# Optimization experiments

Measured on AMD Instinct MI355X. Metric: run time of the kernel, lower is better.

## Reference

```python
import jax, jax.numpy as jnp
import numpy as np

TAU = 2.0
THR = 1.0
ALPHA = 10.0
FLOW_SCALE = 16.0  # 2 ** flow_scale_pow2 (=4)
DECAY = 1.0 - 1.0 / TAU


def conv2d(x, w, b=None, stride=1, pad=0):
    # x: [N,C,H,W], w: [O,I,kh,kw]
    out = jax.lax.conv_general_dilated(
        x, w, (stride, stride), [(pad, pad), (pad, pad)],
        dimension_numbers=('NCHW', 'OIHW', 'NCHW'))
    if b is not None:
        out = out + b[None, :, None, None]
    return out


@jax.custom_vjp
def spike(v):
    return (v > 0).astype(v.dtype)

def _spike_fwd(v):
    return (v > 0).astype(v.dtype), v

def _spike_bwd(v, g):
    s = jax.nn.sigmoid(ALPHA * v)
    return (g * ALPHA * s * (1.0 - s),)

spike.defvjp(_spike_fwd, _spike_bwd)


def lif(x, w, b, mem, stride, pad):
    """Conv + leaky-integrate-fire with soft reset. mem init 0 -> first step mem=cur."""
    cur = conv2d(x, w, b, stride, pad)
    mem = mem * DECAY + cur
    s = spike(mem - THR)
    mem = mem - s * THR
    return s, mem


def up2(x):
    return jnp.repeat(jnp.repeat(x, 2, axis=2), 2, axis=3)


def forward(x, w_e1, b_e1, w_e2, b_e2, w_e3, b_e3, w_d3, b_d3,
            w_d2, b_d2, w_d1, b_d1, w_skip2, w_skip1, w_flow, b_flow):
    N, T, C, H, W = x.shape
    bc = w_e1.shape[0]  # base_ch = 32
    z = lambda c, h, w: jnp.zeros((N, c, h, w), x.dtype)
    init = (
        z(bc, H // 2, W // 2),      # mem_e1
        z(2 * bc, H // 4, W // 4),  # mem_e2
        z(4 * bc, H // 8, W // 8),  # mem_e3
        z(2 * bc, H // 4, W // 4),  # mem_d3
        z(bc, H // 2, W // 2),      # mem_d2
        z(bc, H, W),                # mem_d1
        z(bc, H // 2, W // 2),      # mean_e1 (zeros + /(t+1) rule == None-init)
        z(2 * bc, H // 4, W // 4),  # mean_e2
        z(2, H, W),                 # flow_mean
    )

    def step(carry, inp):
        t, xt = inp
        m1, m2, m3, md3, md2, md1, me1, me2, fm = carry
        s1, m1 = lif(xt, w_e1, b_e1, m1, 2, 2)
        s2, m2 = lif(s1, w_e2, b_e2, m2, 2, 1)
        s3, m3 = lif(s2, w_e3, b_e3, m3, 2, 1)
        tf = (t + 1).astype(xt.dtype)
        me1 = me1 + (s1 - me1) / tf
        me2 = me2 + (s2 - me2) / tf
        d3, md3 = lif(up2(s3), w_d3, b_d3, md3, 1, 1)
        d3 = d3 + conv2d(me2, w_skip2)
        d2, md2 = lif(up2(d3), w_d2, b_d2, md2, 1, 1)
        d2 = d2 + conv2d(me1, w_skip1)
        d1, md1 = lif(up2(d2), w_d1, b_d1, md1, 1, 1)
        flow = conv2d(d1, w_flow, b_flow, 1, 1) * FLOW_SCALE
        fm = fm + (flow - fm) / tf
        return (m1, m2, m3, md3, md2, md1, me1, me2, fm), flow

    _, flows = jax.lax.scan(step, init, (jnp.arange(T), jnp.moveaxis(x, 1, 0)))
    return flows[-1]  # return_last_flow=True -> flow of final timestep [N,2,H,W]


def setup_inputs() -> dict:
    key = jax.random.key(0)
    ks = jax.random.split(key, 16)
    N, T, H, W, bc = 4, 8, 256, 256, 32

    def w(k, o, i, kh, kw):
        return jax.random.normal(k, (o, i, kh, kw), jnp.float32) / np.sqrt(i * kh * kw)

    return {
        'x': jax.random.uniform(ks[0], (N, T, 2, H, W), jnp.float32),
        'w_e1': w(ks[1], bc, 2, 5, 5), 'b_e1': jnp.zeros((bc,), jnp.float32),
        'w_e2': w(ks[2], 2 * bc, bc, 3, 3), 'b_e2': jnp.zeros((2 * bc,), jnp.float32),
        'w_e3': w(ks[3], 4 * bc, 2 * bc, 3, 3), 'b_e3': jnp.zeros((4 * bc,), jnp.float32),
        'w_d3': w(ks[4], 2 * bc, 4 * bc, 3, 3), 'b_d3': jnp.zeros((2 * bc,), jnp.float32),
        'w_d2': w(ks[5], bc, 2 * bc, 3, 3), 'b_d2': jnp.zeros((bc,), jnp.float32),
        'w_d1': w(ks[6], bc, bc, 3, 3), 'b_d1': jnp.zeros((bc,), jnp.float32),
        'w_skip2': w(ks[7], 2 * bc, 2 * bc, 1, 1),
        'w_skip1': w(ks[8], bc, bc, 1, 1),
        'w_flow': w(ks[9], 2, bc, 3, 3), 'b_flow': jnp.zeros((2,), jnp.float32),
    }


def reference(x, w_e1, b_e1, w_e2, b_e2, w_e3, b_e3, w_d3, b_d3,
              w_d2, b_d2, w_d1, b_d1, w_skip2, w_skip1, w_flow, b_flow):
    return forward(x, w_e1, b_e1, w_e2, b_e2, w_e3, b_e3, w_d3, b_d3,
                   w_d2, b_d2, w_d1, b_d1, w_skip2, w_skip1, w_flow, b_flow)
```

## Files before the change

### kernel.cpp

```cpp
#include <hip/hip_runtime.h>
#include <cstdint>
#include <cstddef>


static constexpr float THRc   = 1.0f;
static constexpr float DECAYc = 0.5f;

__device__ __forceinline__ float getc(const float4& v, int k) {
    switch (k & 3) {
        case 0: return v.x;
        case 1: return v.y;
        case 2: return v.z;
        default: return v.w;
    }
}

__global__ __launch_bounds__(256) void prep_collapse(const float* __restrict__ w,
                                                     float* __restrict__ wc, int pairs)
{
    int idx = blockIdx.x * 256 + threadIdx.x;
    if (idx >= pairs) return;
    float a[3][3];
#pragma unroll
    for (int i = 0; i < 3; ++i)
#pragma unroll
        for (int j = 0; j < 3; ++j) a[i][j] = w[idx * 9 + i * 3 + j];
    float rs[2][2][3];
#pragma unroll
    for (int kx = 0; kx < 3; ++kx) {
        rs[0][0][kx] = a[0][kx];
        rs[0][1][kx] = a[1][kx] + a[2][kx];
        rs[1][0][kx] = a[0][kx] + a[1][kx];
        rs[1][1][kx] = a[2][kx];
    }
#pragma unroll
    for (int py = 0; py < 2; ++py)
#pragma unroll
        for (int px = 0; px < 2; ++px)
#pragma unroll
            for (int r = 0; r < 2; ++r) {
                float c0, c1;
                if (px == 0) { c0 = rs[py][r][0];               c1 = rs[py][r][1] + rs[py][r][2]; }
                else         { c0 = rs[py][r][0] + rs[py][r][1]; c1 = rs[py][r][2]; }
                wc[idx * 16 + ((py * 2 + px) * 2 + r) * 2 + 0] = c0;
                wc[idx * 16 + ((py * 2 + px) * 2 + r) * 2 + 1] = c1;
            }
}

template<int IC, int ICC, int OC, int SIH, int SIW, int CPT, int YPB, int OCT,
         int NW, int SKIP_IC, int SKC>
__device__ __forceinline__ void dec_conv_body(
    int b, float* __restrict__ sb,
    const float* __restrict__ in,
    const float* __restrict__ wc,
    const float* __restrict__ bias,
    float* __restrict__ mem,
    float* __restrict__ out,
    const float* __restrict__ skip_in,
    const float* __restrict__ skip_w)
{
    constexpr int NT   = NW * 64;
    constexpr int LPT  = SIW / CPT;
    static_assert((CPT & 1) == 0 && (CPT == 2 || (CPT & 3) == 0), "CPT even");
    static_assert(LPT * YPB == 64, "wave must tile the band");
    static_assert((ICC & 1) == 0, "ICC even");
    constexpr int OC_B = NW * OCT;
    constexpr int NOCB = OC / OC_B;
    constexpr int NYB  = SIH / YPB;
    constexpr int SP   = SIW + 8;
    constexpr int SR   = YPB + 2;
    constexpr int OH   = 2 * SIH, OW = 2 * SIW;
    constexpr int NCH  = IC / ICC;
    constexpr int W4   = SIW / 4;
    constexpr int TILE = ICC * SR * SP;
    constexpr int OROWS = 2 * YPB;
    constexpr int SLOTS = ICC * SR * W4;

    const int ocb = b % NOCB; b /= NOCB;
    const int yb  = b % NYB;  b /= NYB;
    const int n   = b;
    const int y0  = yb * YPB;

    const int lane = threadIdx.x & 63;
    const int wav  = threadIdx.x >> 6;
    const int cl   = lane % LPT;
    const int yp   = lane / LPT;
    const int c0   = cl * CPT;
    const int y    = y0 + yp;

    const int oc0 = __builtin_amdgcn_readfirstlane(ocb * OC_B + wav * OCT);

    int lzero;
    asm volatile("v_mov_b32 %0, 0" : "=v"(lzero));
    const float4* wlane = reinterpret_cast<const float4*>(wc) + lzero;
    const int wbase = oc0 * IC * 4;

    for (int f = threadIdx.x; f < 2 * ICC * SR * 2; f += NT) {
        int side = f & 1;
        int t    = f >> 1;
        int r    = t % SR;
        int tt   = t / SR;
        int ic   = tt % ICC;
        int buf  = tt / ICC;
        sb[buf * TILE + (ic * SR + r) * SP + (side ? (SIW + 4) : 3)] = 0.0f;
    }

    float acc[OCT][2][2 * CPT];
#pragma unroll
    for (int j = 0; j < OCT; ++j) {
        float bv = bias[oc0 + j];
#pragma unroll
        for (int py = 0; py < 2; ++py)
#pragma unroll
            for (int q = 0; q < 2 * CPT; ++q) acc[j][py][q] = bv;
    }

    const float* inn = in + (size_t)n * IC * SIH * SIW;

    float4 wA[OCT * 4], wB[OCT * 4];
    auto wload = [&](int icg, float4* dst) {
#pragma unroll
        for (int j = 0; j < OCT; ++j)
#pragma unroll
            for (int g = 0; g < 4; ++g)
                dst[j * 4 + g] = wlane[wbase + (j * IC + icg) * 4 + g];
    };

    auto stage = [&](int buf, int ch) {
        const float* inb = inn + (size_t)ch * ICC * SIH * SIW;
        float* dst = sb + buf * TILE;
        for (int f = threadIdx.x; f < SLOTS; f += NT) {
            int c4 = f & (W4 - 1);
            int t  = f / W4;
            int r  = t % SR;
            int ic = t / SR;
            int sy = y0 - 1 + r;
            float4 v = make_float4(0.f, 0.f, 0.f, 0.f);
            if (sy >= 0 && sy < SIH)
                v = *reinterpret_cast<const float4*>(
                        inb + (size_t)ic * SIH * SIW + (size_t)sy * SIW + 4 * c4);
            *reinterpret_cast<float4*>(&dst[(ic * SR + r) * SP + 4 + 4 * c4]) = v;
        }
    };

    auto compute = [&](const float* bp, int icl, const float4* w) {
        float s[3][CPT + 2];
#pragma unroll
        for (int r = 0; r < 3; ++r) {
            const int rb = (icl * SR + yp + r) * SP;
            s[r][0] = bp[rb + 3 + c0];
            if constexpr (CPT >= 4) {
#pragma unroll
                for (int v = 0; v < CPT / 4; ++v) {
                    float4 t4 = *reinterpret_cast<const float4*>(&bp[rb + 4 + c0 + 4 * v]);
                    s[r][1 + 4 * v] = t4.x; s[r][2 + 4 * v] = t4.y;
                    s[r][3 + 4 * v] = t4.z; s[r][4 + 4 * v] = t4.w;
                }
            } else {
                float2 t2 = *reinterpret_cast<const float2*>(&bp[rb + 4 + c0]);
                s[r][1] = t2.x; s[r][2] = t2.y;
            }
            s[r][CPT + 1] = bp[rb + 4 + c0 + CPT];
        }
#pragma unroll
        for (int j = 0; j < OCT; ++j)
#pragma unroll
            for (int py = 0; py < 2; ++py)
#pragma unroll
                for (int cc = 0; cc < CPT; ++cc)
#pragma unroll
                    for (int px = 0; px < 2; ++px) {
                        float v = acc[j][py][cc * 2 + px];
#pragma unroll
                        for (int rr = 0; rr < 2; ++rr)
#pragma unroll
                            for (int c2 = 0; c2 < 2; ++c2)
                                v += getc(w[j * 4 + py * 2 + px], rr * 2 + c2)
                                   * s[py + rr][cc + px + c2];
                        acc[j][py][cc * 2 + px] = v;
                    }
    };

    wload(0, wA);
    stage(0, 0);
    __syncthreads();
    for (int ch = 0; ch < NCH; ++ch) {
        if (ch + 1 < NCH) stage((ch + 1) & 1, ch + 1);
        const float* bp = sb + (ch & 1) * TILE;
        const int icg0 = ch * ICC;
        for (int ic = 0; ic < ICC; ic += 2) {
            wload(icg0 + ic + 1, wB);
            compute(bp, ic, wA);
            wload(icg0 + ic + 2, wA);
            compute(bp, ic + 1, wB);
        }
        __syncthreads();
    }

    constexpr int NV = (2 * CPT) / 4;
    float sk[OCT][2][2 * CPT] = {};
    if constexpr (SKIP_IC > 0) {
        constexpr int NSK = SKIP_IC / SKC;
        constexpr int OW4 = OW / 4;
        const float* skn = skip_in + (size_t)n * SKIP_IC * OH * OW;
        for (int sc = 0; sc < NSK; ++sc) {
            if (sc) __syncthreads();
            for (int f = threadIdx.x; f < SKC * OROWS * OW4; f += NT) {
                int c4 = f & (OW4 - 1);
                int t  = f / OW4;
                int r  = t % OROWS;
                int ic = t / OROWS;
                *reinterpret_cast<float4*>(&sb[(ic * OROWS + r) * OW + 4 * c4]) =
                    *reinterpret_cast<const float4*>(
                        skn + ((size_t)(sc * SKC + ic) * OH + 2 * y0 + r) * OW + 4 * c4);
            }
            __syncthreads();
            float wsk[OCT][SKC];
#pragma unroll
            for (int j = 0; j < OCT; ++j)
#pragma unroll
                for (int ic = 0; ic < SKC; ++ic)
                    wsk[j][ic] = skip_w[(size_t)(oc0 + j) * SKIP_IC + sc * SKC + ic];
#pragma unroll
            for (int ic = 0; ic < SKC; ++ic)
#pragma unroll
                for (int py = 0; py < 2; ++py)
#pragma unroll
                    for (int v = 0; v < NV; ++v) {
                        float4 sv = *reinterpret_cast<const float4*>(
                            &sb[(ic * OROWS + 2 * yp + py) * OW + 2 * c0 + 4 * v]);
#pragma unroll
                        for (int j = 0; j < OCT; ++j) {
                            sk[j][py][4 * v + 0] += wsk[j][ic] * sv.x;
                            sk[j][py][4 * v + 1] += wsk[j][ic] * sv.y;
                            sk[j][py][4 * v + 2] += wsk[j][ic] * sv.z;
                            sk[j][py][4 * v + 3] += wsk[j][ic] * sv.w;
                        }
                    }
        }
    }

    const bool wout = (out != nullptr);
#pragma unroll
    for (int j = 0; j < OCT; ++j)
#pragma unroll
        for (int py = 0; py < 2; ++py) {
            size_t ob = (((size_t)n * OC + oc0 + j) * OH + (2 * y + py)) * OW + 2 * c0;
#pragma unroll
            for (int v = 0; v < NV; ++v) {
                float4 mv = *reinterpret_cast<const float4*>(&mem[ob + 4 * v]);
                float4 ov, nm;
                float m0 = mv.x * DECAYc + acc[j][py][4 * v + 0];
                float m1 = mv.y * DECAYc + acc[j][py][4 * v + 1];
                float m2 = mv.z * DECAYc + acc[j][py][4 * v + 2];
                float m3 = mv.w * DECAYc + acc[j][py][4 * v + 3];
                float s0 = (m0 - THRc) > 0.0f ? 1.0f : 0.0f;
                float s1 = (m1 - THRc) > 0.0f ? 1.0f : 0.0f;
                float s2 = (m2 - THRc) > 0.0f ? 1.0f : 0.0f;
                float s3 = (m3 - THRc) > 0.0f ? 1.0f : 0.0f;
                nm.x = m0 - s0 * THRc; nm.y = m1 - s1 * THRc;
                nm.z = m2 - s2 * THRc; nm.w = m3 - s3 * THRc;
                *reinterpret_cast<float4*>(&mem[ob + 4 * v]) = nm;
                if (wout) {
                    ov.x = s0 + sk[j][py][4 * v + 0];
                    ov.y = s1 + sk[j][py][4 * v + 1];
                    ov.z = s2 + sk[j][py][4 * v + 2];
                    ov.w = s3 + sk[j][py][4 * v + 3];
                    *reinterpret_cast<float4*>(&out[ob + 4 * v]) = ov;
                }
            }
        }
}

template<int IC, int ICC, int OC, int IH, int IW, int K, int CPT, int LPT, int OCT, bool DO_MEAN>
__device__ __forceinline__ void enc_conv_body(
    int b, float* __restrict__ sb,
    const float* __restrict__ in, int in_nstride,
    const float* __restrict__ wgt, const float* __restrict__ bias,
    float* __restrict__ mem, float* __restrict__ out,
    const float* __restrict__ mean_in, float* __restrict__ mean_out, float inv_tf)
{
    constexpr int P    = K / 2;
    constexpr int OH   = IH / 2, OW = IW / 2;
    constexpr int SPr  = 4 + IW + P;
    constexpr int SP   = (SPr + 3) & ~3;
    constexpr int OC_B = 4 * OCT;
    constexpr int NOCB = OC / OC_B;
    constexpr int RL   = 2 * CPT + 2 * P - 1;
    constexpr int NCH  = IC / ICC;
    constexpr int W4   = IW / 4;
    static_assert(LPT * CPT == OW, "lanes x CPT must cover OW");
    static_assert((ICC & (ICC - 1)) == 0, "ICC pow2");

    const int ocb = b % NOCB; b /= NOCB;
    const int y   = b % OH;   b /= OH;
    const int n   = b;

    const int lane = threadIdx.x & 63;
    const int wav  = threadIdx.x >> 6;
    const int x0   = (lane % LPT) * CPT;
    const int oc0  = __builtin_amdgcn_readfirstlane(ocb * OC_B + wav * OCT);

    for (int f = threadIdx.x; f < K * ICC * 2 * P; f += 256) {
        int h  = f % (2 * P);
        int t  = f / (2 * P);
        int ic = t & (ICC - 1);
        int r  = t / ICC;
        int col = (h < P) ? (4 - P + h) : (4 + IW + h - P);
        sb[(r * ICC + ic) * SP + col] = 0.0f;
    }

    float acc[OCT][CPT];
#pragma unroll
    for (int j = 0; j < OCT; ++j) {
        float bv = bias[oc0 + j];
#pragma unroll
        for (int cc = 0; cc < CPT; ++cc) acc[j][cc] = bv;
    }

    const float* inn = in + (size_t)n * (size_t)in_nstride;

    for (int ch = 0; ch < NCH; ++ch) {
        __syncthreads();
        const float* inb = inn + (size_t)ch * ICC * IH * IW;
        constexpr int SLOTS = K * ICC * W4;
        for (int f = threadIdx.x; f < SLOTS; f += 256) {
            int c4 = f & (W4 - 1);
            int t  = f / W4;
            int ic = t & (ICC - 1);
            int r  = t / ICC;
            int sy = 2 * y - P + r;
            float4 v = make_float4(0.f, 0.f, 0.f, 0.f);
            if (sy >= 0 && sy < IH)
                v = *reinterpret_cast<const float4*>(
                        inb + (size_t)ic * IH * IW + (size_t)sy * IW + 4 * c4);
            *reinterpret_cast<float4*>(&sb[(r * ICC + ic) * SP + 4 + 4 * c4]) = v;
        }
        __syncthreads();
        for (int ic = 0; ic < ICC; ++ic) {
            float s[K][RL];
#pragma unroll
            for (int r = 0; r < K; ++r)
#pragma unroll
                for (int k = 0; k < RL; ++k)
                    s[r][k] = sb[(r * ICC + ic) * SP + 4 - P + 2 * x0 + k];
            const float* wp = wgt + ((size_t)oc0 * IC + ch * ICC + ic) * (K * K);
#pragma unroll
            for (int j = 0; j < OCT; ++j) {
                float wv[K * K];
#pragma unroll
                for (int k = 0; k < K * K; ++k) wv[k] = wp[(size_t)j * IC * K * K + k];
#pragma unroll
                for (int cc = 0; cc < CPT; ++cc)
#pragma unroll
                    for (int ky = 0; ky < K; ++ky)
#pragma unroll
                        for (int kx = 0; kx < K; ++kx)
                            acc[j][cc] += wv[ky * K + kx] * s[ky][2 * cc + kx];
            }
        }
    }

    if (lane < LPT) {
#pragma unroll
        for (int j = 0; j < OCT; ++j) {
            size_t ob = (((size_t)n * OC + oc0 + j) * OH + y) * OW + x0;
#pragma unroll
            for (int cc = 0; cc < CPT; ++cc) {
                float m  = mem[ob + cc] * DECAYc + acc[j][cc];
                float sp = (m - THRc) > 0.0f ? 1.0f : 0.0f;
                mem[ob + cc] = m - sp * THRc;
                if constexpr (DO_MEAN) {
                    float mv = mean_in[ob + cc];
                    mean_out[ob + cc] = mv + (sp - mv) * inv_tf;
                }
                out[ob + cc] = sp;
            }
        }
    }
}

template<int IC, int ICC, int OC, int IH, int IW, int CPT, int LPT, int OCT, bool DO_MEAN>
__device__ __forceinline__ void enc_convdb_body(
    int b, float* __restrict__ sb,
    const float* __restrict__ in, int in_nstride,
    const float* __restrict__ wgt, const float* __restrict__ bias,
    float* __restrict__ mem, float* __restrict__ out,
    const float* __restrict__ mean_in, float* __restrict__ mean_out, float inv_tf)
{
    constexpr int K    = 3;
    constexpr int P    = 1;
    constexpr int OH   = IH / 2, OW = IW / 2;
    constexpr int SPr  = 4 + IW + P;
    constexpr int SP   = (SPr + 3) & ~3;
    constexpr int OC_B = 4 * OCT;
    constexpr int NOCB = OC / OC_B;
    constexpr int RL   = 2 * CPT + 2 * P - 1;
    constexpr int NCH  = IC / ICC;
    constexpr int W4   = IW / 4;
    constexpr int TILE = K * ICC * SP;
    constexpr int SLOTS = K * ICC * W4;
    static_assert(LPT * CPT == OW, "lanes x CPT must cover OW");
    static_assert((ICC & (ICC - 1)) == 0, "ICC pow2");
    static_assert(NCH >= 2, "dbuf needs >=2 chunks");

    const int ocb = b % NOCB; b /= NOCB;
    const int y   = b % OH;   b /= OH;
    const int n   = b;

    const int lane = threadIdx.x & 63;
    const int wav  = threadIdx.x >> 6;
    const int x0   = (lane % LPT) * CPT;
    const int oc0  = __builtin_amdgcn_readfirstlane(ocb * OC_B + wav * OCT);

    for (int f = threadIdx.x; f < 2 * K * ICC * 2 * P; f += 256) {
        int h   = f % (2 * P);
        int t   = f / (2 * P);
        int ic  = t & (ICC - 1);
        int t2  = t / ICC;
        int r   = t2 % K;
        int buf = t2 / K;
        int col = (h < P) ? (4 - P + h) : (4 + IW + h - P);
        sb[buf * TILE + (r * ICC + ic) * SP + col] = 0.0f;
    }

    float acc[OCT][CPT];
#pragma unroll
    for (int j = 0; j < OCT; ++j) {
        float bv = bias[oc0 + j];
#pragma unroll
        for (int cc = 0; cc < CPT; ++cc) acc[j][cc] = bv;
    }

    const float* inn = in + (size_t)n * (size_t)in_nstride;

    auto stage = [&](int buf, int ch) {
        const float* inb = inn + (size_t)ch * ICC * IH * IW;
        float* dst = sb + buf * TILE;
        for (int f = threadIdx.x; f < SLOTS; f += 256) {
            int c4 = f & (W4 - 1);
            int t  = f / W4;
            int ic = t & (ICC - 1);
            int r  = t / ICC;
            int sy = 2 * y - P + r;
            float4 v = make_float4(0.f, 0.f, 0.f, 0.f);
            if (sy >= 0 && sy < IH)
                v = *reinterpret_cast<const float4*>(
                        inb + (size_t)ic * IH * IW + (size_t)sy * IW + 4 * c4);
            *reinterpret_cast<float4*>(&dst[(r * ICC + ic) * SP + 4 + 4 * c4]) = v;
        }
    };

    stage(0, 0);
    __syncthreads();
    for (int ch = 0; ch < NCH; ++ch) {
        if (ch + 1 < NCH) stage((ch + 1) & 1, ch + 1);
        const float* bp = sb + (ch & 1) * TILE;
        for (int ic = 0; ic < ICC; ++ic) {
            float s[K][RL];
#pragma unroll
            for (int r = 0; r < K; ++r)
#pragma unroll
                for (int k = 0; k < RL; ++k)
                    s[r][k] = bp[(r * ICC + ic) * SP + 4 - P + 2 * x0 + k];
            const float* wp = wgt + ((size_t)oc0 * IC + ch * ICC + ic) * (K * K);
#pragma unroll
            for (int j = 0; j < OCT; ++j) {
                float wv[K * K];
#pragma unroll
                for (int k = 0; k < K * K; ++k) wv[k] = wp[(size_t)j * IC * K * K + k];
#pragma unroll
                for (int cc = 0; cc < CPT; ++cc)
#pragma unroll
                    for (int ky = 0; ky < K; ++ky)
#pragma unroll
                        for (int kx = 0; kx < K; ++kx)
                            acc[j][cc] += wv[ky * K + kx] * s[ky][2 * cc + kx];
            }
        }
        __syncthreads();
    }

    if (lane < LPT) {
#pragma unroll
        for (int j = 0; j < OCT; ++j) {
            size_t ob = (((size_t)n * OC + oc0 + j) * OH + y) * OW + x0;
#pragma unroll
            for (int cc = 0; cc < CPT; ++cc) {
                float m  = mem[ob + cc] * DECAYc + acc[j][cc];
                float sp = (m - THRc) > 0.0f ? 1.0f : 0.0f;
                mem[ob + cc] = m - sp * THRc;
                if constexpr (DO_MEAN) {
                    float mv = mean_in[ob + cc];
                    mean_out[ob + cc] = mv + (sp - mv) * inv_tf;
                }
                out[ob + cc] = sp;
            }
        }
    }
}

template<int IC, int ICC, int OC, int IH, int IW, int K, int CPT, int LPT, int OCT,
         bool DO_MEAN, int SMEMW>
__global__ __launch_bounds__(256) void enc_conv_k(
    const float* in, int ns, const float* wgt, const float* bias,
    float* mem, float* out, const float* mean_in, float* mean_out, float inv_tf)
{
    __shared__ __align__(16) float smem[SMEMW];
    enc_conv_body<IC, ICC, OC, IH, IW, K, CPT, LPT, OCT, DO_MEAN>(
        (int)blockIdx.x, smem, in, ns, wgt, bias, mem, out, mean_in, mean_out, inv_tf);
}

template<int IC, int ICC, int OC, int IH, int IW, int CPT, int LPT, int OCT,
         bool DO_MEAN, int SMEMW>
__global__ __launch_bounds__(256) void enc_convdb_k(
    const float* in, int ns, const float* wgt, const float* bias,
    float* mem, float* out, const float* mean_in, float* mean_out, float inv_tf)
{
    __shared__ __align__(16) float smem[SMEMW];
    enc_convdb_body<IC, ICC, OC, IH, IW, CPT, LPT, OCT, DO_MEAN>(
        (int)blockIdx.x, smem, in, ns, wgt, bias, mem, out, mean_in, mean_out, inv_tf);
}

__global__ __launch_bounds__(256) void fused_d3_e1(
    const float* din, const float* dwc, const float* dbias, float* dmem,
    float* dout, const float* dskip_in, const float* dskip_w,
    const float* ein, int ens, const float* ew, const float* ebias,
    float* emem, float* eout, const float* emean_in, float* emean_out, float einv)
{
    __shared__ __align__(16) float smem[7680];
    int b = (int)blockIdx.x;
    if (b < 512)
        dec_conv_body<128, 16, 64, 32, 32, 2, 4, 1, 4, 64, 8>(
            b, smem, din, dwc, dbias, dmem, dout, dskip_in, dskip_w);
    else
        enc_conv_body<2, 2, 32, 256, 256, 5, 2, 64, 2, true>(
            b - 512, smem, ein, ens, ew, ebias, emem, eout, emean_in, emean_out, einv);
}

__global__ __launch_bounds__(256) void fused_d2_e2(
    const float* din, const float* dwc, const float* dbias, float* dmem,
    float* dout, const float* dskip_in, const float* dskip_w,
    const float* ein, int ens, const float* ew, const float* ebias,
    float* emem, float* eout, const float* emean_in, float* emean_out, float einv)
{
    __shared__ __align__(16) float smem[9216];
    int b = (int)blockIdx.x;
    if (b < 512)
        dec_conv_body<64, 16, 32, 64, 64, 2, 2, 2, 4, 32, 8>(
            b, smem, din, dwc, dbias, dmem, dout, dskip_in, dskip_w);
    else
        enc_convdb_body<32, 8, 64, 128, 128, 1, 64, 2, true>(
            b - 512, smem, ein, ens, ew, ebias, emem, eout, emean_in, emean_out, einv);
}

__global__ __launch_bounds__(256) void fused_d1_e3(
    const float* din, const float* dwc, const float* dbias, float* dmem,
    float* dout,
    const float* ein, int ens, const float* ew, const float* ebias,
    float* emem, float* eout, float einv)
{
    __shared__ __align__(16) float smem[8704];
    int b = (int)blockIdx.x;
    if (b < 1024)
        dec_conv_body<32, 8, 32, 128, 128, 4, 2, 2, 4, 0, 1>(
            b, smem, din, dwc, dbias, dmem, dout, nullptr, nullptr);
    else
        enc_convdb_body<64, 16, 128, 64, 64, 1, 32, 4, false>(
            b - 1024, smem, ein, ens, ew, ebias, emem, eout, nullptr, nullptr, einv);
}

template<int IC, int OC, int IH, int IW, int OH, int OW,
         int K, int STRIDE, int PAD, bool UP2, int SKIP_IC,
         bool DO_LIF, bool DO_MEAN>
__global__ __launch_bounds__(256) void conv_fused(
    const float* __restrict__ in, int in_nstride,
    const float* __restrict__ wgt,
    const float* __restrict__ bias,
    float* __restrict__ mem,
    float* __restrict__ out,
    const float* __restrict__ skip_in,
    const float* __restrict__ skip_w,
    float* __restrict__ mean,
    float inv_tf, float outscale)
{
    constexpr int VEC  = 4;
    constexpr int OWV  = OW / VEC;
    constexpr int WSZ  = IC * K * K;
    constexpr int SIH  = UP2 ? IH / 2 : IH;
    constexpr int SIW  = UP2 ? IW / 2 : IW;
    constexpr int RLEN = (VEC - 1) * STRIDE + K;

    __shared__ float sw[WSZ];

    const int bstart = blockIdx.x * 256;
    const int oc = (bstart / (OH * OWV)) % OC;

    for (int i = threadIdx.x; i < WSZ; i += 256) sw[i] = wgt[oc * WSZ + i];
    __syncthreads();

    const int idx = bstart + threadIdx.x;
    const int wx  = idx % OWV;
    int tt        = idx / OWV;
    const int oy  = tt % OH; tt /= OH;
    tt /= OC;
    const int n   = tt;
    const int ox0 = wx * VEC;

    const float bv = bias ? bias[oc] : 0.0f;
    float acc[VEC];
#pragma unroll
    for (int v = 0; v < VEC; ++v) acc[v] = bv;

    const float* inn = in + (size_t)n * (size_t)in_nstride;

    for (int ic = 0; ic < IC; ++ic) {
        const float* inc = inn + (size_t)ic * (SIH * SIW);
#pragma unroll
        for (int ky = 0; ky < K; ++ky) {
            const int uy = oy * STRIDE + ky - PAD;
            const bool rowok = (uy >= 0) & (uy < IH);
            int sy = UP2 ? (uy >> 1) : uy;
            sy = sy < 0 ? 0 : (sy > SIH - 1 ? SIH - 1 : sy);
            const float* __restrict__ row = inc + (size_t)sy * SIW;

            float r[RLEN];
#pragma unroll
            for (int j = 0; j < RLEN; ++j) {
                const int ux = ox0 * STRIDE - PAD + j;
                const bool ok = rowok & (ux >= 0) & (ux < IW);
                int sx = UP2 ? (ux >> 1) : ux;
                sx = sx < 0 ? 0 : (sx > SIW - 1 ? SIW - 1 : sx);
                r[j] = ok ? row[sx] : 0.0f;
            }
#pragma unroll
            for (int kx = 0; kx < K; ++kx) {
                const float wv = sw[(ic * K + ky) * K + kx];
#pragma unroll
                for (int v = 0; v < VEC; ++v)
                    acc[v] += r[v * STRIDE + kx] * wv;
            }
        }
    }

    const size_t obase = ((((size_t)n * OC + oc) * OH) + oy) * (size_t)OW + ox0;
#pragma unroll
    for (int v = 0; v < VEC; ++v) out[obase + v] = acc[v] * outscale;
}

extern "C" void kernel_launch(void* const* d_in, const int* in_sizes, int n_in,
                              void* d_out, int out_size, void* d_ws, size_t ws_size,
                              hipStream_t stream)
{
    const float* x     = (const float*)d_in[0];
    const float* w_e1  = (const float*)d_in[1];
    const float* b_e1  = (const float*)d_in[2];
    const float* w_e2  = (const float*)d_in[3];
    const float* b_e2  = (const float*)d_in[4];
    const float* w_e3  = (const float*)d_in[5];
    const float* b_e3  = (const float*)d_in[6];
    const float* w_d3  = (const float*)d_in[7];
    const float* b_d3  = (const float*)d_in[8];
    const float* w_d2  = (const float*)d_in[9];
    const float* b_d2  = (const float*)d_in[10];
    const float* w_d1  = (const float*)d_in[11];
    const float* b_d1  = (const float*)d_in[12];
    const float* w_sk2 = (const float*)d_in[13];
    const float* w_sk1 = (const float*)d_in[14];
    const float* w_fl  = (const float*)d_in[15];
    const float* b_fl  = (const float*)d_in[16];
    float* outp = (float*)d_out;

    float* ws = (float*)d_ws;
    size_t off = 0;
    auto alloc = [&](size_t nelem) { float* p = ws + off; off += nelem; return p; };

    float* m1   = alloc(4UL * 32 * 128 * 128);
    float* m2   = alloc(4UL * 64 * 64 * 64);
    float* m3   = alloc(4UL * 128 * 32 * 32);
    float* md3  = alloc(4UL * 64 * 64 * 64);
    float* md2  = alloc(4UL * 32 * 128 * 128);
    float* md1  = alloc(4UL * 32 * 256 * 256);
    float* me1a = alloc(4UL * 32 * 128 * 128);
    float* me1b = alloc(4UL * 32 * 128 * 128);
    float* me2  = alloc(4UL * 64 * 64 * 64);
    const size_t zcount = off;
    float* s1  = alloc(4UL * 32 * 128 * 128);
    float* s2  = alloc(4UL * 64 * 64 * 64);
    float* s3  = alloc(4UL * 128 * 32 * 32);
    float* d3a = alloc(4UL * 64 * 64 * 64);
    float* d2a = alloc(4UL * 32 * 128 * 128);
    float* d1a = alloc(4UL * 32 * 256 * 256);
    float* wc3 = alloc(64UL * 128 * 16 + 64);
    float* wc2 = alloc(32UL * 64 * 16 + 64);
    float* wc1 = alloc(32UL * 32 * 16 + 64);
    (void)ws_size; (void)in_sizes; (void)n_in; (void)out_size;

    hipMemsetAsync(d_ws, 0, zcount * sizeof(float), stream);

    prep_collapse<<<(64 * 128 + 255) / 256, 256, 0, stream>>>(w_d3, wc3, 64 * 128);
    prep_collapse<<<(32 * 64 + 255) / 256, 256, 0, stream>>>(w_d2, wc2, 32 * 64);
    prep_collapse<<<(32 * 32 + 255) / 256, 256, 0, stream>>>(w_d1, wc1, 32 * 32);

    float* me1buf[2] = { me1a, me1b };

    enc_conv_k<2, 2, 32, 256, 256, 5, 2, 64, 2, true, 2640>
        <<<4 * 128 * 4, 256, 0, stream>>>(x, 8 * 2 * 256 * 256, w_e1, b_e1,
                                          m1, s1, me1buf[0], me1buf[1], 1.0f);
    enc_convdb_k<32, 8, 64, 128, 128, 1, 64, 2, true, 6528>
        <<<4 * 64 * 8, 256, 0, stream>>>(s1, 32 * 128 * 128, w_e2, b_e2,
                                         m2, s2, me2, me2, 1.0f);
    enc_convdb_k<64, 16, 128, 64, 64, 1, 32, 4, false, 6912>
        <<<4 * 32 * 8, 256, 0, stream>>>(s2, 64 * 64 * 64, w_e3, b_e3,
                                         m3, s3, nullptr, nullptr, 1.0f);

    for (int t = 0; t < 8; ++t) {
        const int  t1 = t + 1;
        const bool he = t1 < 8;
        const int  xc = he ? t1 : 7;
        const float einv = 1.0f / (float)(t1 + 1);
        const float* xt1 = x + (size_t)xc * 2 * 256 * 256;
        const float* d2skip = me1buf[1 - (t & 1)];
        const float* e1in  = me1buf[t1 & 1];
        float*       e1out = me1buf[1 - (t1 & 1)];

        fused_d3_e1<<<he ? 2560 : 512, 256, 0, stream>>>(
            s3, wc3, b_d3, md3, d3a, me2, w_sk2,
            xt1, 8 * 2 * 256 * 256, w_e1, b_e1, m1, s1, e1in, e1out, einv);
        fused_d2_e2<<<he ? 2560 : 512, 256, 0, stream>>>(
            d3a, wc2, b_d2, md2, d2a, d2skip, w_sk1,
            s1, 32 * 128 * 128, w_e2, b_e2, m2, s2, me2, me2, einv);
        fused_d1_e3<<<he ? 2048 : 1024, 256, 0, stream>>>(
            d2a, wc1, b_d1, md1, (t == 7) ? d1a : nullptr,
            s2, 64 * 64 * 64, w_e3, b_e3, m3, s3, einv);
    }

    conv_fused<32, 2, 256, 256, 256, 256, 3, 1, 1, false, 0, false, false>
        <<<512, 256, 0, stream>>>(d1a, 32 * 256 * 256, w_fl, b_fl,
                                  nullptr, outp, nullptr, nullptr, nullptr, 1.0f, 16.0f);
}
```

Baseline: 2.339 ms.

## Re-pair decoder and encoder stages across timesteps in fused kernels

Changes how the next timestep's encoder work is co-scheduled with the current decoder. e3 now runs as its own kernel, d3 runs alone, d2 is fused with e1, and d1 is fused with e2. Previously the pairs were d3+e1, d2+e2 and d1+e3. Adds a launch-bounds occupancy hint of 3 blocks on the fused kernels. This raises the launch count from three to four per step, so each fused launch can better balance heavy and light work, at the cost of an extra launch and serialized small e3/d3 kernels.

```diff
diff --git a/kernel.cpp b/kernel.cpp
--- a/kernel.cpp
+++ b/kernel.cpp
@@ -522,23 +522,18 @@
         (int)blockIdx.x, smem, in, ns, wgt, bias, mem, out, mean_in, mean_out, inv_tf);
 }
 
-__global__ __launch_bounds__(256) void fused_d3_e1(
-    const float* din, const float* dwc, const float* dbias, float* dmem,
-    float* dout, const float* dskip_in, const float* dskip_w,
-    const float* ein, int ens, const float* ew, const float* ebias,
-    float* emem, float* eout, const float* emean_in, float* emean_out, float einv)
-{
-    __shared__ __align__(16) float smem[7680];
-    int b = (int)blockIdx.x;
-    if (b < 512)
-        dec_conv_body<128, 16, 64, 32, 32, 2, 4, 1, 4, 64, 8>(
-            b, smem, din, dwc, dbias, dmem, dout, dskip_in, dskip_w);
-    else
-        enc_conv_body<2, 2, 32, 256, 256, 5, 2, 64, 2, true>(
-            b - 512, smem, ein, ens, ew, ebias, emem, eout, emean_in, emean_out, einv);
-}
-
-__global__ __launch_bounds__(256) void fused_d2_e2(
+template<int IC, int ICC, int OC, int SIH, int SIW, int CPT, int YPB, int OCT,
+         int NW, int SKIP_IC, int SKC, int SMEMW>
+__global__ __launch_bounds__(NW * 64) void dec_conv_k(
+    const float* in, const float* wc, const float* bias,
+    float* mem, float* out, const float* skip_in, const float* skip_w)
+{
+    __shared__ __align__(16) float smem[SMEMW];
+    dec_conv_body<IC, ICC, OC, SIH, SIW, CPT, YPB, OCT, NW, SKIP_IC, SKC>(
+        (int)blockIdx.x, smem, in, wc, bias, mem, out, skip_in, skip_w);
+}
+
+__global__ __launch_bounds__(256, 3) void fused_d2_e1(
     const float* din, const float* dwc, const float* dbias, float* dmem,
     float* dout, const float* dskip_in, const float* dskip_w,
     const float* ein, int ens, const float* ew, const float* ebias,
@@ -550,15 +545,15 @@
         dec_conv_body<64, 16, 32, 64, 64, 2, 2, 2, 4, 32, 8>(
             b, smem, din, dwc, dbias, dmem, dout, dskip_in, dskip_w);
     else
-        enc_convdb_body<32, 8, 64, 128, 128, 1, 64, 2, true>(
+        enc_conv_body<2, 2, 32, 256, 256, 5, 2, 64, 2, true>(
             b - 512, smem, ein, ens, ew, ebias, emem, eout, emean_in, emean_out, einv);
 }
 
-__global__ __launch_bounds__(256) void fused_d1_e3(
+__global__ __launch_bounds__(256, 3) void fused_d1_e2(
     const float* din, const float* dwc, const float* dbias, float* dmem,
     float* dout,
     const float* ein, int ens, const float* ew, const float* ebias,
-    float* emem, float* eout, float einv)
+    float* emem, float* eout, const float* emean_in, float* emean_out, float einv)
 {
     __shared__ __align__(16) float smem[8704];
     int b = (int)blockIdx.x;
@@ -566,8 +561,8 @@
         dec_conv_body<32, 8, 32, 128, 128, 4, 2, 2, 4, 0, 1>(
             b, smem, din, dwc, dbias, dmem, dout, nullptr, nullptr);
     else
-        enc_convdb_body<64, 16, 128, 64, 64, 1, 32, 4, false>(
-            b - 1024, smem, ein, ens, ew, ebias, emem, eout, nullptr, nullptr, einv);
+        enc_convdb_body<32, 8, 64, 128, 128, 1, 64, 2, true>(
+            b - 1024, smem, ein, ens, ew, ebias, emem, eout, emean_in, emean_out, einv);
 }
 
 template<int IC, int OC, int IH, int IW, int OH, int OW,
@@ -710,9 +705,6 @@
     enc_convdb_k<32, 8, 64, 128, 128, 1, 64, 2, true, 6528>
         <<<4 * 64 * 8, 256, 0, stream>>>(s1, 32 * 128 * 128, w_e2, b_e2,
                                          m2, s2, me2, me2, 1.0f);
-    enc_convdb_k<64, 16, 128, 64, 64, 1, 32, 4, false, 6912>
-        <<<4 * 32 * 8, 256, 0, stream>>>(s2, 64 * 64 * 64, w_e3, b_e3,
-                                         m3, s3, nullptr, nullptr, 1.0f);
 
     for (int t = 0; t < 8; ++t) {
         const int  t1 = t + 1;
@@ -720,19 +712,22 @@
         const int  xc = he ? t1 : 7;
         const float einv = 1.0f / (float)(t1 + 1);
         const float* xt1 = x + (size_t)xc * 2 * 256 * 256;
-        const float* d2skip = me1buf[1 - (t & 1)];
-        const float* e1in  = me1buf[t1 & 1];
-        float*       e1out = me1buf[1 - (t1 & 1)];
-
-        fused_d3_e1<<<he ? 2560 : 512, 256, 0, stream>>>(
-            s3, wc3, b_d3, md3, d3a, me2, w_sk2,
-            xt1, 8 * 2 * 256 * 256, w_e1, b_e1, m1, s1, e1in, e1out, einv);
-        fused_d2_e2<<<he ? 2560 : 512, 256, 0, stream>>>(
-            d3a, wc2, b_d2, md2, d2a, d2skip, w_sk1,
+        const float* me1_t = me1buf[1 - (t & 1)];
+        float*       e1out = me1buf[t & 1];
+        const float inv_tf = 1.0f / (float)(t + 1);
+        (void)inv_tf;
+
+        enc_convdb_k<64, 16, 128, 64, 64, 1, 32, 4, false, 6912>
+            <<<4 * 32 * 8, 256, 0, stream>>>(s2, 64 * 64 * 64, w_e3, b_e3,
+                                             m3, s3, nullptr, nullptr, 1.0f);
+        dec_conv_k<128, 16, 64, 32, 32, 2, 4, 1, 4, 64, 8, 7680>
+            <<<4 * 8 * 16, 256, 0, stream>>>(s3, wc3, b_d3, md3, d3a, me2, w_sk2);
+        fused_d2_e1<<<he ? 2560 : 512, 256, 0, stream>>>(
+            d3a, wc2, b_d2, md2, d2a, me1_t, w_sk1,
+            xt1, 8 * 2 * 256 * 256, w_e1, b_e1, m1, s1, me1_t, e1out, einv);
+        fused_d1_e2<<<he ? 3072 : 1024, 256, 0, stream>>>(
+            d2a, wc1, b_d1, md1, (t == 7) ? d1a : nullptr,
             s1, 32 * 128 * 128, w_e2, b_e2, m2, s2, me2, me2, einv);
-        fused_d1_e3<<<he ? 2048 : 1024, 256, 0, stream>>>(
-            d2a, wc1, b_d1, md1, (t == 7) ? d1a : nullptr,
-            s2, 64 * 64 * 64, w_e3, b_e3, m3, s3, einv);
     }
 
     conv_fused<32, 2, 256, 256, 256, 256, 3, 1, 1, false, 0, false, false>
```

Measured after the change: 2.322 ms. About the same (-0.7%).
